# Kernel tuning notes

Hardware: AMD Instinct MI355X
Metric: run time of the kernel (lower is better)

Reference implementation:

```python
import jax, jax.numpy as jnp
import numpy as np

T, B, I, Hd = 512, 64, 128, 1024
SIGMA = 0.01


def setup_inputs() -> dict:
    key = jax.random.key(0)
    k1, k2, k3 = jax.random.split(key, 3)
    X = jax.random.normal(k1, (T, B, I), dtype=jnp.float32)
    W_ih = jax.random.normal(k2, (I, Hd), dtype=jnp.float32) * SIGMA
    W_hh = jax.random.normal(k3, (Hd, Hd), dtype=jnp.float32) * SIGMA
    b_h = jnp.zeros((Hd,), dtype=jnp.float32)
    H0 = jnp.zeros((B, Hd), dtype=jnp.float32)
    return {"X": X, "W_ih": W_ih, "W_hh": W_hh, "b_h": b_h, "H0": H0}


def reference(X, W_ih, W_hh, b_h, H0):
    # Pre-batch the input projection across all timesteps (same math,
    # one big GEMM instead of T small ones): [T,B,I] @ [I,H] -> [T,B,H]
    Xp = jnp.einsum("tbi,ih->tbh", X, W_ih) + b_h

    def step(H, xp_t):
        H_new = jnp.tanh(xp_t + H @ W_hh)
        return H_new, H_new

    H_final, states = jax.lax.scan(step, H0, Xp)
    # states: [T, B, H] (stack of per-timestep hidden states), H_final: [B, H]
    return states, H_final
```

## Files before the change

kernel.cpp:

```cpp
#include <hip/hip_runtime.h>
#include <hip/hip_bf16.h>
#include <stdint.h>

#define T_STEPS 512
#define BATCH   64
#define IN_DIM  128
#define HID     1024
#define KTOT    (HID + IN_DIM)
#define NWAVES  4
#define THREADS (NWAVES * 64)

#define NGRP    2
#define GB      32
#define NSL     32
#define NCOLS   32
#define NKK     36
#define WBYTES  (KTOT * NCOLS * 2)
#define HBYTES  (GB * HID * 2)
#define LDSB    (WBYTES + HBYTES)

#define RING    16
#define DCLR    4
#define SLOT    (BATCH * HID)
#define SENT    0x7F7F7F7F
#define NFLAGS  (NGRP * NSL * NWAVES * NSL)

typedef float f32x4 __attribute__((ext_vector_type(4)));
typedef int   i32x4 __attribute__((ext_vector_type(4)));
typedef short s16x8 __attribute__((ext_vector_type(8)));
typedef uint32_t u32x2 __attribute__((ext_vector_type(2)));

#define MFMA16 __builtin_amdgcn_mfma_f32_16x16x32_bf16

__device__ __forceinline__ uint32_t cvt_pk_bf16(float a, float b) {
    uint32_t r;
    asm("v_cvt_pk_bf16_f32 %0, %1, %2" : "=v"(r) : "v"(a), "v"(b));
    return r;
}

union frag_u { uint32_t u[4]; s16x8 s; };

__device__ __forceinline__ s16x8 pack_bf16x8(f32x4 a, f32x4 b) {
    frag_u f;
    f.u[0] = cvt_pk_bf16(a.x, a.y);
    f.u[1] = cvt_pk_bf16(a.z, a.w);
    f.u[2] = cvt_pk_bf16(b.x, b.y);
    f.u[3] = cvt_pk_bf16(b.z, b.w);
    return f.s;
}

__device__ __forceinline__ uint16_t f32_to_bf16(float v) {
    uint32_t u = __builtin_bit_cast(uint32_t, v);
    return (uint16_t)((u + 0x7FFFu + ((u >> 16) & 1u)) >> 16);
}

__device__ __forceinline__ float tanh_fast(float x) {
    float e = __expf(2.0f * x);
    return 1.0f - 2.0f * __builtin_amdgcn_rcpf(e + 1.0f);
}

__device__ __forceinline__ int imax(int a, int b) { return a > b ? a : b; }
__device__ __forceinline__ int max4(f32x4 v) {
    i32x4 a = __builtin_bit_cast(i32x4, v);
    return imax(imax(a.x, a.y), imax(a.z, a.w));
}

__global__ void rnn_init_kernel(const float* __restrict__ H0,
                                uint16_t* __restrict__ comm) {
    int i = blockIdx.x * 256 + threadIdx.x;
    for (int e = i; e < SLOT; e += 64 * 256)
        comm[e] = f32_to_bf16(H0[e]);
}

__global__ __launch_bounds__(THREADS, 1)
void rnn_seq_kernel(const float* __restrict__ X, const float* __restrict__ Wih,
                    const float* __restrict__ Whh, const float* __restrict__ bh,
                    float* __restrict__ out, uint16_t* __restrict__ comm,
                    int* __restrict__ flags2)
{
    extern __shared__ char lds[];
    char* Hl = lds + WBYTES;

    const int tid = threadIdx.x;
    const int wg  = blockIdx.x;
    const int g   = wg >> 5;
    const int p   = wg & 31;
    const int hc0 = p * NCOLS;
    const int bg0 = g * GB;

    for (int e = tid; e < NCOLS * KTOT; e += THREADS) {
        int c2 = e & 31;
        int k  = e >> 5;
        int n  = c2 >> 4, c = c2 & 15;
        float w = (k < HID) ? Whh[(size_t)k * HID + hc0 + c2]
                            : Wih[(size_t)(k - HID) * HID + hc0 + c2];
        uint32_t off = ((uint32_t)(n * NKK + (k >> 5)) << 10)
                     + (((k >> 3) & 3) << 8) + (c << 4) + ((k & 7) << 1);
        *(uint16_t*)(lds + off) = f32_to_bf16(w);
    }
    __syncthreads();

    const int lane = tid & 63, wv = tid >> 6;
    const int cb = lane & 15, kg = lane >> 4;
    const int bt = wv >> 1, ct = wv & 1;
    const int b  = bg0 + bt * 16 + cb;
    const int h  = hc0 + ct * 16 + kg * 4;
    const char* wfb = lds + (size_t)ct * NKK * 1024 + lane * 16;
    const f32x4 bv = *(const f32x4*)(bh + h);

    const int* fpoll = flags2 + (wg * NWAVES + wv) * NSL + (lane & 31);
    int* fst = flags2 + ((g * NSL + (lane & 31)) * NWAVES + wv) * NSL + p;

    uint16_t* wb = comm + (size_t)b * HID + h;
    float* ob = out + (size_t)b * HID + h;

    const int r = bt * 16 + cb;
    const uint32_t abase = (uint32_t)r * 2048 + (uint32_t)kg * 16;
    const uint32_t aswz  = (uint32_t)(r & 7) << 4;

    const size_t gstage = (size_t)bg0 * HID;
    u32x2 sentv; sentv.x = SENT; sentv.y = SENT;

    for (int t = 0; t < T_STEPS; ++t) {
        f32x4 acc0 = {0.f,0.f,0.f,0.f}, acc1 = {0.f,0.f,0.f,0.f};

        const float* xrow = X + ((size_t)t * BATCH + b) * IN_DIM;
        #pragma unroll
        for (int kk = 0; kk < 4; ++kk) {
            int kidx = kk * 32 + kg * 8;
            f32x4 f0 = *(const f32x4*)(xrow + kidx);
            f32x4 f1 = *(const f32x4*)(xrow + kidx + 4);
            s16x8 xf = pack_bf16x8(f0, f1);
            s16x8 wf = *(const s16x8*)(wfb + (32 + kk) * 1024);
            if (kk & 1) acc1 = MFMA16(wf, xf, acc1, 0, 0, 0);
            else        acc0 = MFMA16(wf, xf, acc0, 0, 0, 0);
        }
        __builtin_amdgcn_sched_barrier(0);

        if (t > 0) {
            for (;;) {
                int f;
                asm volatile("global_load_dword %0, %1, off sc0 sc1\n\t"
                             "s_waitcnt vmcnt(0)"
                             : "=v"(f) : "v"(fpoll) : "memory");
                if (__all(f >= t)) break;
            }
        }
        asm volatile("s_waitcnt vmcnt(0)" ::: "memory");
        __builtin_amdgcn_sched_barrier(0);

        const char* gb = (const char*)(comm + (size_t)(t & (RING - 1)) * SLOT
                                       + gstage) + tid * 16;
        f32x4 L[16];
        for (;;) {
            #pragma unroll
            for (int i = 0; i < 16; ++i)
                asm volatile("global_load_dwordx4 %0, %1, off sc0 sc1"
                             : "=v"(L[i]) : "v"(gb + (size_t)i * 4096) : "memory");
            asm volatile("s_waitcnt vmcnt(0)" ::: "memory");
            __builtin_amdgcn_sched_barrier(0);
            int m = (int)0x80000000;
            #pragma unroll
            for (int i = 0; i < 16; ++i) m = imax(m, max4(L[i]));
            if (__all(m != (int)SENT)) break;
        }
        #pragma unroll
        for (int i = 0; i < 16; ++i) {
            int j = i * 256 + tid;
            uint32_t off = ((uint32_t)j * 16) ^ ((((uint32_t)j >> 7) & 7) << 4);
            *(f32x4*)(Hl + off) = L[i];
        }
        __syncthreads();

        #pragma unroll
        for (int kk = 0; kk < 32; ++kk) {
            s16x8 af = *(const s16x8*)(Hl + ((abase + (uint32_t)kk * 64) ^ aswz));
            s16x8 wf = *(const s16x8*)(wfb + kk * 1024);
            if (kk & 1) acc1 = MFMA16(wf, af, acc1, 0, 0, 0);
            else        acc0 = MFMA16(wf, af, acc0, 0, 0, 0);
        }

        float t0 = tanh_fast(acc0[0] + acc1[0] + bv.x);
        float t1 = tanh_fast(acc0[1] + acc1[1] + bv.y);
        float t2 = tanh_fast(acc0[2] + acc1[2] + bv.z);
        float t3 = tanh_fast(acc0[3] + acc1[3] + bv.w);

        u32x2 cd;
        cd.x = cvt_pk_bf16(t0, t1);
        cd.y = cvt_pk_bf16(t2, t3);
        uint16_t* pw = wb + (size_t)((t + 1) & (RING - 1)) * SLOT;
        asm volatile("global_store_dwordx2 %0, %1, off sc0 sc1"
                     :: "v"(pw), "v"(cd) : "memory");
        __syncthreads();
        if (lane < 32) {
            int fv = t + 1;
            asm volatile("global_store_dword %0, %1, off sc0 sc1"
                         :: "v"(fst), "v"(fv) : "memory");
        }
        {
            uint16_t* pc = wb + (size_t)((t + 1 + DCLR) & (RING - 1)) * SLOT;
            asm volatile("global_store_dwordx2 %0, %1, off sc0 sc1"
                         :: "v"(pc), "v"(sentv) : "memory");
        }

        f32x4 vo; vo.x = t0; vo.y = t1; vo.z = t2; vo.w = t3;
        *(f32x4*)(ob + (size_t)t * BATCH * HID) = vo;
        if (t == T_STEPS - 1)
            *(f32x4*)(ob + (size_t)T_STEPS * BATCH * HID) = vo;
    }
}

extern "C" void kernel_launch(void* const* d_in, const int* in_sizes, int n_in,
                              void* d_out, int out_size, void* d_ws, size_t ws_size,
                              hipStream_t stream) {
    (void)in_sizes; (void)n_in; (void)out_size; (void)ws_size;
    const float* X   = (const float*)d_in[0];
    const float* Wih = (const float*)d_in[1];
    const float* Whh = (const float*)d_in[2];
    const float* bh  = (const float*)d_in[3];
    const float* H0  = (const float*)d_in[4];
    float* out = (float*)d_out;

    uint16_t* comm = (uint16_t*)d_ws;
    int* flags2 = (int*)((char*)d_ws + (size_t)RING * SLOT * 2);

    hipFuncSetAttribute((const void*)rnn_seq_kernel,
                        hipFuncAttributeMaxDynamicSharedMemorySize, LDSB);

    hipMemsetAsync(comm, 0x7F, (size_t)RING * SLOT * 2, stream);
    hipMemsetAsync(flags2, 0, NFLAGS * sizeof(int), stream);
    hipLaunchKernelGGL(rnn_init_kernel, dim3(64), dim3(256), 0, stream, H0, comm);
    hipLaunchKernelGGL(rnn_seq_kernel, dim3(NGRP * NSL), dim3(THREADS), LDSB, stream,
                       X, Wih, Whh, bh, out, comm, flags2);
}
```

Before: 2.058 ms.

## Keep recurrent weights in registers and retile to four batch groups of sixteen

The workload is redistributed to 4 batch groups × 16 column slices, with each workgroup covering 64 hidden columns for 16 batch rows. Each wave now keeps its 36 weight fragments in registers instead of reading them from LDS every step. The hidden-state staging buffer is double-buffered in LDS and the post-store __syncthreads is removed, so per-wave flags signal readiness directly. This cuts LDS traffic and the per-step barrier, at the cost of heavy register pressure and more flag polling per wave.

```diff
diff --git a/kernel.cpp b/kernel.cpp
--- a/kernel.cpp
+++ b/kernel.cpp
@@ -10,20 +10,19 @@
 #define NWAVES  4
 #define THREADS (NWAVES * 64)
 
-#define NGRP    2
-#define GB      32
-#define NSL     32
-#define NCOLS   32
-#define NKK     36
-#define WBYTES  (KTOT * NCOLS * 2)
-#define HBYTES  (GB * HID * 2)
-#define LDSB    (WBYTES + HBYTES)
+#define NGRP    4
+#define NSL     16
+#define NB      16
+#define NKH     32
+#define NKX     4
+#define HBUF    32768
+#define LDSB    73728
 
 #define RING    16
 #define DCLR    4
 #define SLOT    (BATCH * HID)
 #define SENT    0x7F7F7F7F
-#define NFLAGS  (NGRP * NSL * NWAVES * NSL)
+#define NFLAGS  (NGRP * NSL * NWAVES * 64)
 
 typedef float f32x4 __attribute__((ext_vector_type(4)));
 typedef int   i32x4 __attribute__((ext_vector_type(4)));
@@ -79,46 +78,51 @@
                     int* __restrict__ flags2)
 {
     extern __shared__ char lds[];
-    char* Hl = lds + WBYTES;
 
     const int tid = threadIdx.x;
-    const int wg  = blockIdx.x;
-    const int g   = wg >> 5;
-    const int p   = wg & 31;
-    const int hc0 = p * NCOLS;
-    const int bg0 = g * GB;
-
-    for (int e = tid; e < NCOLS * KTOT; e += THREADS) {
-        int c2 = e & 31;
-        int k  = e >> 5;
-        int n  = c2 >> 4, c = c2 & 15;
-        float w = (k < HID) ? Whh[(size_t)k * HID + hc0 + c2]
-                            : Wih[(size_t)(k - HID) * HID + hc0 + c2];
-        uint32_t off = ((uint32_t)(n * NKK + (k >> 5)) << 10)
-                     + (((k >> 3) & 3) << 8) + (c << 4) + ((k & 7) << 1);
-        *(uint16_t*)(lds + off) = f32_to_bf16(w);
-    }
-    __syncthreads();
-
+    const int grp = blockIdx.x >> 4;
+    const int p   = blockIdx.x & 15;
     const int lane = tid & 63, wv = tid >> 6;
     const int cb = lane & 15, kg = lane >> 4;
-    const int bt = wv >> 1, ct = wv & 1;
-    const int b  = bg0 + bt * 16 + cb;
-    const int h  = hc0 + ct * 16 + kg * 4;
-    const char* wfb = lds + (size_t)ct * NKK * 1024 + lane * 16;
+    const int hc0 = p * 64;
+    const int b   = grp * NB + cb;
+
+    s16x8 wreg[36];
+    #pragma unroll
+    for (int half = 0; half < 2; ++half) {
+        for (int e = tid; e < 32 * KTOT; e += THREADS) {
+            int c2 = e & 31;
+            int k  = e >> 5;
+            int hcol = hc0 + half * 32 + c2;
+            float w = (k < HID) ? Whh[(size_t)k * HID + hcol]
+                                : Wih[(size_t)(k - HID) * HID + hcol];
+            uint32_t off = ((uint32_t)((c2 >> 4) * 36 + (k >> 5)) << 10)
+                         + (((k >> 3) & 3) << 8) + ((c2 & 15) << 4) + ((k & 7) << 1);
+            *(uint16_t*)(lds + off) = f32_to_bf16(w);
+        }
+        __syncthreads();
+        if ((wv >> 1) == half) {
+            const char* base = lds + (size_t)(wv & 1) * 36 * 1024 + lane * 16;
+            #pragma unroll
+            for (int kk = 0; kk < 36; ++kk)
+                wreg[kk] = *(const s16x8*)(base + (size_t)kk * 1024);
+        }
+        __syncthreads();
+    }
+
+    const int h = hc0 + wv * 16 + kg * 4;
     const f32x4 bv = *(const f32x4*)(bh + h);
 
-    const int* fpoll = flags2 + (wg * NWAVES + wv) * NSL + (lane & 31);
-    int* fst = flags2 + ((g * NSL + (lane & 31)) * NWAVES + wv) * NSL + p;
+    const int* fpoll = flags2 + ((grp * NSL + p) * NWAVES + wv) * 64 + lane;
+    int* fst = flags2 + ((grp * NSL + (lane & 15)) * NWAVES + (lane >> 4)) * 64
+             + (p * NWAVES + wv);
 
     uint16_t* wb = comm + (size_t)b * HID + h;
     float* ob = out + (size_t)b * HID + h;
 
-    const int r = bt * 16 + cb;
-    const uint32_t abase = (uint32_t)r * 2048 + (uint32_t)kg * 16;
-    const uint32_t aswz  = (uint32_t)(r & 7) << 4;
-
-    const size_t gstage = (size_t)bg0 * HID;
+    const size_t ssrc = (size_t)(grp * NB + (tid & 15)) * HID
+                      + ((tid >> 4) & 3) * 8 + (tid >> 6) * 32;
+
     u32x2 sentv; sentv.x = SENT; sentv.y = SENT;
 
     for (int t = 0; t < T_STEPS; ++t) {
@@ -126,14 +130,13 @@
 
         const float* xrow = X + ((size_t)t * BATCH + b) * IN_DIM;
         #pragma unroll
-        for (int kk = 0; kk < 4; ++kk) {
+        for (int kk = 0; kk < NKX; ++kk) {
             int kidx = kk * 32 + kg * 8;
             f32x4 f0 = *(const f32x4*)(xrow + kidx);
             f32x4 f1 = *(const f32x4*)(xrow + kidx + 4);
             s16x8 xf = pack_bf16x8(f0, f1);
-            s16x8 wf = *(const s16x8*)(wfb + (32 + kk) * 1024);
-            if (kk & 1) acc1 = MFMA16(wf, xf, acc1, 0, 0, 0);
-            else        acc0 = MFMA16(wf, xf, acc0, 0, 0, 0);
+            if (kk & 1) acc1 = MFMA16(wreg[32 + kk], xf, acc1, 0, 0, 0);
+            else        acc0 = MFMA16(wreg[32 + kk], xf, acc0, 0, 0, 0);
         }
         __builtin_amdgcn_sched_barrier(0);
 
@@ -146,38 +149,35 @@
                 if (__all(f >= t)) break;
             }
         }
-        asm volatile("s_waitcnt vmcnt(0)" ::: "memory");
         __builtin_amdgcn_sched_barrier(0);
 
-        const char* gb = (const char*)(comm + (size_t)(t & (RING - 1)) * SLOT
-                                       + gstage) + tid * 16;
-        f32x4 L[16];
+        char* Hb = lds + (size_t)(t & 1) * HBUF;
+        const char* gsrc = (const char*)(comm + (size_t)(t & (RING - 1)) * SLOT
+                                         + ssrc);
+        f32x4 L[8];
         for (;;) {
             #pragma unroll
-            for (int i = 0; i < 16; ++i)
+            for (int i = 0; i < 8; ++i)
                 asm volatile("global_load_dwordx4 %0, %1, off sc0 sc1"
-                             : "=v"(L[i]) : "v"(gb + (size_t)i * 4096) : "memory");
+                             : "=v"(L[i]) : "v"(gsrc + (size_t)i * 256) : "memory");
             asm volatile("s_waitcnt vmcnt(0)" ::: "memory");
             __builtin_amdgcn_sched_barrier(0);
             int m = (int)0x80000000;
             #pragma unroll
-            for (int i = 0; i < 16; ++i) m = imax(m, max4(L[i]));
+            for (int i = 0; i < 8; ++i) m = imax(m, max4(L[i]));
             if (__all(m != (int)SENT)) break;
         }
         #pragma unroll
-        for (int i = 0; i < 16; ++i) {
-            int j = i * 256 + tid;
-            uint32_t off = ((uint32_t)j * 16) ^ ((((uint32_t)j >> 7) & 7) << 4);
-            *(f32x4*)(Hl + off) = L[i];
-        }
+        for (int i = 0; i < 8; ++i)
+            *(f32x4*)(Hb + tid * 16 + i * 4096) = L[i];
         __syncthreads();
 
+        const char* hfb = Hb + lane * 16;
         #pragma unroll
-        for (int kk = 0; kk < 32; ++kk) {
-            s16x8 af = *(const s16x8*)(Hl + ((abase + (uint32_t)kk * 64) ^ aswz));
-            s16x8 wf = *(const s16x8*)(wfb + kk * 1024);
-            if (kk & 1) acc1 = MFMA16(wf, af, acc1, 0, 0, 0);
-            else        acc0 = MFMA16(wf, af, acc0, 0, 0, 0);
+        for (int kk = 0; kk < NKH; ++kk) {
+            s16x8 af = *(const s16x8*)(hfb + (size_t)kk * 1024);
+            if (kk & 1) acc1 = MFMA16(wreg[kk], af, acc1, 0, 0, 0);
+            else        acc0 = MFMA16(wreg[kk], af, acc0, 0, 0, 0);
         }
 
         float t0 = tanh_fast(acc0[0] + acc1[0] + bv.x);
@@ -191,8 +191,7 @@
         uint16_t* pw = wb + (size_t)((t + 1) & (RING - 1)) * SLOT;
         asm volatile("global_store_dwordx2 %0, %1, off sc0 sc1"
                      :: "v"(pw), "v"(cd) : "memory");
-        __syncthreads();
-        if (lane < 32) {
+        {
             int fv = t + 1;
             asm volatile("global_store_dword %0, %1, off sc0 sc1"
                          :: "v"(fst), "v"(fv) : "memory");
```

Result: no change. 2.060 ms (+0.1%).
